# Optimization experiments

Measured on AMD Instinct MI355X. Metric: run time of the kernel, lower is better.

Reference implementation:

```python
import jax, jax.numpy as jnp
import numpy as np

N_NODES = 50000
N_EDGES = 800000
IN_CH = 128
HID = 128


def setup_inputs() -> dict:
    key = jax.random.key(0)
    ks = jax.random.split(key, 16)
    inp = {
        "x": jax.random.normal(ks[0], (N_NODES, IN_CH), dtype=jnp.float32),
        "edge_index": jax.random.randint(ks[1], (2, N_EDGES), 0, N_NODES, dtype=jnp.int64),
        "batch_size": 1024,
    }
    dims = [(IN_CH, HID), (HID, HID), (HID, HID)]
    for i, (din, dout) in enumerate(dims):
        s = 1.0 / np.sqrt(din)
        inp[f"W_l{i}"] = jax.random.uniform(ks[2 + 4 * i], (dout, din), jnp.float32, -s, s)
        inp[f"b_l{i}"] = jax.random.uniform(ks[3 + 4 * i], (dout,), jnp.float32, -s, s)
        inp[f"W_r{i}"] = jax.random.uniform(ks[4 + 4 * i], (dout, din), jnp.float32, -s, s)
        inp[f"a{i}"] = jnp.full((dout,), 0.25, dtype=jnp.float32)  # PReLU slope
    return inp


def _sage_prelu(x, src, dst, W_l, b_l, W_r, a):
    # mean aggregation of source messages at target nodes
    msg_sum = jax.ops.segment_sum(x[src], dst, num_segments=N_NODES)  # [N, din]
    deg = jax.ops.segment_sum(jnp.ones((src.shape[0],), x.dtype), dst, num_segments=N_NODES)
    agg = msg_sum / jnp.maximum(deg, 1.0)[:, None]
    out = agg @ W_l.T + b_l + x @ W_r.T  # lin_l(aggr) + lin_r(x), bias on lin_l only
    return jnp.where(out > 0, out, a * out)  # per-channel PReLU


def reference(x, edge_index, batch_size, W_l0, b_l0, W_r0, a0, W_l1, b_l1, W_r1, a1, W_l2, b_l2, W_r2, a2):
    src, dst = edge_index[0], edge_index[1]
    x = _sage_prelu(x, src, dst, W_l0, b_l0, W_r0, a0)
    x = _sage_prelu(x, src, dst, W_l1, b_l1, W_r1, a1)
    x = _sage_prelu(x, src, dst, W_l2, b_l2, W_r2, a2)
    return x[:batch_size]
```

## Files before the change

kernel.cpp:

```cpp
#include <hip/hip_runtime.h>

#define NN 50000
#define NE 800000
#define C 128
#define CAP 64
#define EB2 ((NE / 2 + 255) / 256)
#define SPLITB 1563
#define WB 96
#define EB4 ((NE / 4 + 255) / 256)
#define ASTRIDE 136

typedef __attribute__((ext_vector_type(8))) short bf16x8;
typedef __attribute__((ext_vector_type(4))) float f32x4;
typedef unsigned short ushort;

__device__ inline ushort bf16_rn(float f) {
    unsigned u = __builtin_bit_cast(unsigned, f);
    u += 0x7FFF + ((u >> 16) & 1);
    return (ushort)(u >> 16);
}
__device__ inline void split_bf16(float f, ushort& hi, ushort& lo) {
    hi = bf16_rn(f);
    float hif = __builtin_bit_cast(float, (unsigned)hi << 16);
    lo = bf16_rn(f - hif);
}
__device__ inline float bf_lo(unsigned u) { return __builtin_bit_cast(float, u << 16); }
__device__ inline float bf_hi(unsigned u) { return __builtin_bit_cast(float, u & 0xFFFF0000u); }


__global__ __launch_bounds__(256)
void prep_kernel(const int* __restrict__ dst, const float* __restrict__ x,
                 const float* __restrict__ W0, const float* __restrict__ W1,
                 const float* __restrict__ W2, const float* __restrict__ W3,
                 const float* __restrict__ W4, const float* __restrict__ W5,
                 int* __restrict__ deg, int* __restrict__ pos,
                 ushort* __restrict__ Ah, ushort* __restrict__ Al,
                 ushort* __restrict__ Wh, ushort* __restrict__ Wl) {
    int t = threadIdx.x;
    if (blockIdx.x < EB2) {
        int e0 = (blockIdx.x * 256 + t) * 2;
        if (e0 < NE) {
            int2 d2 = *(const int2*)(dst + e0);
            int p0 = atomicAdd(&deg[d2.x], 1);
            int p1 = atomicAdd(&deg[d2.y], 1);
            *(int2*)(pos + e0) = make_int2(p0, p1);
        }
    } else if (blockIdx.x < EB2 + SPLITB) {
        int tid = (blockIdx.x - EB2) * 256 + t;
        const int total = NN * C / 4;
        for (int i = tid; i < total; i += SPLITB * 256) {
            f32x4 v = ((const f32x4*)x)[i];
            ushort h0, h1, h2, h3, l0, l1, l2, l3;
            split_bf16(v.x, h0, l0);
            split_bf16(v.y, h1, l1);
            split_bf16(v.z, h2, l2);
            split_bf16(v.w, h3, l3);
            *(uint2*)(Ah + (size_t)i * 4) = make_uint2((unsigned)h0 | ((unsigned)h1 << 16),
                                                       (unsigned)h2 | ((unsigned)h3 << 16));
            *(uint2*)(Al + (size_t)i * 4) = make_uint2((unsigned)l0 | ((unsigned)l1 << 16),
                                                       (unsigned)l2 | ((unsigned)l3 << 16));
        }
    } else {
        const float* Ws[6] = {W0, W1, W2, W3, W4, W5};
        int i = (blockIdx.x - EB2 - SPLITB) * 256 + t;
        int mat = i >> 12;
        f32x4 v = ((const f32x4*)Ws[mat])[i & 4095];
        ushort h0, h1, h2, h3, l0, l1, l2, l3;
        split_bf16(v.x, h0, l0);
        split_bf16(v.y, h1, l1);
        split_bf16(v.z, h2, l2);
        split_bf16(v.w, h3, l3);
        *(uint2*)(Wh + (size_t)i * 4) = make_uint2((unsigned)h0 | ((unsigned)h1 << 16),
                                                   (unsigned)h2 | ((unsigned)h3 << 16));
        *(uint2*)(Wl + (size_t)i * 4) = make_uint2((unsigned)l0 | ((unsigned)l1 << 16),
                                                   (unsigned)l2 | ((unsigned)l3 << 16));
    }
}


__global__ __launch_bounds__(256)
void fill_kernel(const int* __restrict__ src, const int* __restrict__ dst,
                 const int* __restrict__ pos, int* __restrict__ col) {
    int e0 = (blockIdx.x * 256 + threadIdx.x) * 4;
    if (e0 >= NE) return;
    int4 da = *(const int4*)(dst + e0);
    int4 sa = *(const int4*)(src + e0);
    int4 pa = *(const int4*)(pos + e0);
    if (pa.x < CAP) col[da.x * CAP + pa.x] = sa.x;
    if (pa.y < CAP) col[da.y * CAP + pa.y] = sa.y;
    if (pa.z < CAP) col[da.z * CAP + pa.z] = sa.z;
    if (pa.w < CAP) col[da.w * CAP + pa.w] = sa.w;
}


__global__ __launch_bounds__(256)
void mark_kernel(const int* __restrict__ deg, const int* __restrict__ col,
                 int* __restrict__ needed, int rows_out) {
    int i = blockIdx.x * 256 + threadIdx.x;
    int n = i / CAP;
    int s = i - n * CAP;
    if (n >= rows_out) return;
    if (s == 0) needed[n] = 1;
    if (s < min(deg[n], CAP)) needed[col[n * CAP + s]] = 1;
}


__global__ __launch_bounds__(256)
void compact_kernel(const int* __restrict__ needed, int* __restrict__ list,
                    int* __restrict__ cnt) {
    int i = blockIdx.x * 256 + threadIdx.x;
    if (i < NN && needed[i]) {
        int p = atomicAdd(cnt, 1);
        list[p] = i;
    }
}


__global__ __launch_bounds__(256)
void agg_kernel(const ushort* __restrict__ xh, const int* __restrict__ deg,
                const int* __restrict__ col,
                const int* __restrict__ list, const int* __restrict__ countp,
                ushort* __restrict__ aggh, ushort* __restrict__ aggl, int nodes) {
    int i = (blockIdx.x * blockDim.x + threadIdx.x) >> 6;
    int lane = threadIdx.x & 63;
    int cnt = list ? *countp : nodes;
    if (i >= cnt) return;
    int node = list ? list[i] : i;
    int quad = lane >> 4;
    int ql   = lane & 15;
    int d = min(deg[node], CAP);
    int start = node * CAP;
    int end = start + d;
    const uint4* xr = (const uint4*)xh;
    float a0=0,a1=0,a2=0,a3=0,a4=0,a5=0,a6=0,a7=0;
    int e = start;
    for (; e + 7 < end; e += 8) {
        int i0 = col[e + quad];
        int i1 = col[e + 4 + quad];
        uint4 u0 = xr[(size_t)i0 * 16 + ql];
        uint4 u1 = xr[(size_t)i1 * 16 + ql];
        a0 += bf_lo(u0.x) + bf_lo(u1.x); a1 += bf_hi(u0.x) + bf_hi(u1.x);
        a2 += bf_lo(u0.y) + bf_lo(u1.y); a3 += bf_hi(u0.y) + bf_hi(u1.y);
        a4 += bf_lo(u0.z) + bf_lo(u1.z); a5 += bf_hi(u0.z) + bf_hi(u1.z);
        a6 += bf_lo(u0.w) + bf_lo(u1.w); a7 += bf_hi(u0.w) + bf_hi(u1.w);
    }
    for (; e + 3 < end; e += 4) {
        uint4 u = xr[(size_t)col[e + quad] * 16 + ql];
        a0 += bf_lo(u.x); a1 += bf_hi(u.x);
        a2 += bf_lo(u.y); a3 += bf_hi(u.y);
        a4 += bf_lo(u.z); a5 += bf_hi(u.z);
        a6 += bf_lo(u.w); a7 += bf_hi(u.w);
    }
    int rem = end - e;
    if (quad < rem) {
        uint4 u = xr[(size_t)col[e + quad] * 16 + ql];
        a0 += bf_lo(u.x); a1 += bf_hi(u.x);
        a2 += bf_lo(u.y); a3 += bf_hi(u.y);
        a4 += bf_lo(u.z); a5 += bf_hi(u.z);
        a6 += bf_lo(u.w); a7 += bf_hi(u.w);
    }
    a0 += __shfl_xor(a0, 16, 64); a0 += __shfl_xor(a0, 32, 64);
    a1 += __shfl_xor(a1, 16, 64); a1 += __shfl_xor(a1, 32, 64);
    a2 += __shfl_xor(a2, 16, 64); a2 += __shfl_xor(a2, 32, 64);
    a3 += __shfl_xor(a3, 16, 64); a3 += __shfl_xor(a3, 32, 64);
    a4 += __shfl_xor(a4, 16, 64); a4 += __shfl_xor(a4, 32, 64);
    a5 += __shfl_xor(a5, 16, 64); a5 += __shfl_xor(a5, 32, 64);
    a6 += __shfl_xor(a6, 16, 64); a6 += __shfl_xor(a6, 32, 64);
    a7 += __shfl_xor(a7, 16, 64); a7 += __shfl_xor(a7, 32, 64);
    if (quad == 0) {
        float inv = 1.0f / (float)max(d, 1);
        float m[8] = {a0*inv, a1*inv, a2*inv, a3*inv, a4*inv, a5*inv, a6*inv, a7*inv};
        ushort h[8], o[8];
        #pragma unroll
        for (int j = 0; j < 8; ++j) split_bf16(m[j], h[j], o[j]);
        size_t off = (size_t)node * C + ql * 8;
        *(uint4*)(aggh + off) = make_uint4((unsigned)h[0] | ((unsigned)h[1] << 16),
                                           (unsigned)h[2] | ((unsigned)h[3] << 16),
                                           (unsigned)h[4] | ((unsigned)h[5] << 16),
                                           (unsigned)h[6] | ((unsigned)h[7] << 16));
        *(uint4*)(aggl + off) = make_uint4((unsigned)o[0] | ((unsigned)o[1] << 16),
                                           (unsigned)o[2] | ((unsigned)o[3] << 16),
                                           (unsigned)o[4] | ((unsigned)o[5] << 16),
                                           (unsigned)o[6] | ((unsigned)o[7] << 16));
    }
}


__global__ __launch_bounds__(256, 3)
void gemm_kernel(const ushort* __restrict__ Ah, const ushort* __restrict__ Al,
                 const ushort* __restrict__ Xh, const ushort* __restrict__ Xl,
                 const ushort* __restrict__ Wlh, const ushort* __restrict__ Wll,
                 const ushort* __restrict__ Wrh, const ushort* __restrict__ Wrl,
                 const float* __restrict__ bl, const float* __restrict__ slope,
                 const int* __restrict__ list, const int* __restrict__ countp,
                 float* __restrict__ outf, ushort* __restrict__ outh,
                 ushort* __restrict__ outl, int rows) {
    __shared__ ushort Ahi[64 * ASTRIDE];
    __shared__ ushort Alo[64 * ASTRIDE];
    int t = threadIdx.x;
    int lane = t & 63;
    int w = t >> 6;
    int l = lane & 15;
    int q = lane >> 4;
    int row0 = blockIdx.x * 64;
    int cnt = list ? min(*countp, rows) : rows;
    if (row0 >= cnt) return;

    f32x4 acc[4][2];
    #pragma unroll
    for (int mt = 0; mt < 4; ++mt)
        #pragma unroll
        for (int nt = 0; nt < 2; ++nt)
            acc[mt][nt] = (f32x4){0.f, 0.f, 0.f, 0.f};

    #pragma unroll
    for (int mat = 0; mat < 2; ++mat) {
        const ushort* WH = mat ? Wrh : Wlh;
        const ushort* WL = mat ? Wrl : Wll;
        const ushort* Ph = mat ? Xh : Ah;
        const ushort* Pl = mat ? Xl : Al;

        bf16x8 bhi[2][4], blo[2][4];
        #pragma unroll
        for (int nt = 0; nt < 2; ++nt) {
            int n = w * 32 + nt * 16 + l;
            const ushort* wp = WH + (size_t)n * C + q * 8;
            const ushort* wq = WL + (size_t)n * C + q * 8;
            #pragma unroll
            for (int kb = 0; kb < 4; ++kb) {
                bhi[nt][kb] = *(const bf16x8*)(wp + kb * 32);
                blo[nt][kb] = *(const bf16x8*)(wq + kb * 32);
            }
        }

        __syncthreads();
        int ar = t >> 2;
        int aq = t & 3;
        int ridx = min(row0 + ar, cnt - 1);
        int r = list ? list[ridx] : ridx;
        ushort* dh = Ahi + ar * ASTRIDE + aq * 32;
        ushort* dl = Alo + ar * ASTRIDE + aq * 32;
        const ushort* ph = Ph + (size_t)r * C + aq * 32;
        const ushort* pl = Pl + (size_t)r * C + aq * 32;
        #pragma unroll
        for (int i = 0; i < 4; ++i) {
            *(uint4*)(dh + i * 8) = *(const uint4*)(ph + i * 8);
            *(uint4*)(dl + i * 8) = *(const uint4*)(pl + i * 8);
        }
        __syncthreads();

        #pragma unroll
        for (int kb = 0; kb < 4; ++kb) {
            #pragma unroll
            for (int mt = 0; mt < 4; ++mt) {
                int off = (mt * 16 + l) * ASTRIDE + kb * 32 + q * 8;
                bf16x8 ahi = *(const bf16x8*)(Ahi + off);
                bf16x8 alo = *(const bf16x8*)(Alo + off);
                #pragma unroll
                for (int nt = 0; nt < 2; ++nt) {
                    acc[mt][nt] = __builtin_amdgcn_mfma_f32_16x16x32_bf16(ahi, bhi[nt][kb], acc[mt][nt], 0, 0, 0);
                    acc[mt][nt] = __builtin_amdgcn_mfma_f32_16x16x32_bf16(alo, bhi[nt][kb], acc[mt][nt], 0, 0, 0);
                    acc[mt][nt] = __builtin_amdgcn_mfma_f32_16x16x32_bf16(ahi, blo[nt][kb], acc[mt][nt], 0, 0, 0);
                }
            }
        }
    }

    #pragma unroll
    for (int nt = 0; nt < 2; ++nt) {
        int n = w * 32 + nt * 16 + l;
        float b = bl[n], s = slope[n];
        #pragma unroll
        for (int mt = 0; mt < 4; ++mt) {
            #pragma unroll
            for (int rg = 0; rg < 4; ++rg) {
                int ridx = row0 + mt * 16 + q * 4 + rg;
                if (ridx < cnt) {
                    int r = list ? list[ridx] : ridx;
                    float v = acc[mt][nt][rg] + b;
                    v = v > 0.f ? v : s * v;
                    if (outf) {
                        outf[(size_t)r * C + n] = v;
                    } else {
                        ushort hh, ll;
                        split_bf16(v, hh, ll);
                        outh[(size_t)r * C + n] = hh;
                        outl[(size_t)r * C + n] = ll;
                    }
                }
            }
        }
    }
}


extern "C" void kernel_launch(void* const* d_in, const int* in_sizes, int n_in,
                              void* d_out, int out_size, void* d_ws, size_t ws_size,
                              hipStream_t stream) {
    const float* x   = (const float*)d_in[0];
    const int*   src = (const int*)d_in[1];
    const int*   dst = src + NE;
    const float* Wl[3] = {(const float*)d_in[3], (const float*)d_in[7],  (const float*)d_in[11]};
    const float* bl[3] = {(const float*)d_in[4], (const float*)d_in[8],  (const float*)d_in[12]};
    const float* Wr[3] = {(const float*)d_in[5], (const float*)d_in[9],  (const float*)d_in[13]};
    const float* sl[3] = {(const float*)d_in[6], (const float*)d_in[10], (const float*)d_in[14]};

    int*   deg     = (int*)d_ws;
    int*   needed  = deg + 50016;
    int*   cnt     = needed + 50016;
    int*   pos     = cnt + 16;
    int*   col     = pos + 800000;
    int*   list    = col + NN * CAP;
    ushort* Whs    = (ushort*)(list + 50016);
    ushort* Wls    = Whs + 6 * 16384;
    ushort* Gh     = Wls + 6 * 16384;
    ushort* Gl     = Gh + (size_t)NN * C;
    ushort* Ah     = Gl + (size_t)NN * C;
    ushort* Al     = Ah + (size_t)NN * C;
    ushort* Bh     = Al + (size_t)NN * C;
    ushort* Bl     = Bh + (size_t)NN * C;

    int rows_out = out_size / C;

    hipMemsetAsync(deg, 0, (2 * 50016 + 16) * sizeof(int), stream);

    prep_kernel<<<EB2 + SPLITB + WB, 256, 0, stream>>>(
        dst, x, Wl[0], Wr[0], Wl[1], Wr[1], Wl[2], Wr[2],
        deg, pos, Ah, Al, Whs, Wls);
    fill_kernel<<<EB4, 256, 0, stream>>>(src, dst, pos, col);

    mark_kernel<<<(rows_out * CAP + 255) / 256, 256, 0, stream>>>(deg, col, needed, rows_out);
    compact_kernel<<<(NN + 255) / 256, 256, 0, stream>>>(needed, list, cnt);

    agg_kernel<<<(NN + 3) / 4, 256, 0, stream>>>(Ah, deg, col, nullptr, nullptr, Gh, Gl, NN);
    gemm_kernel<<<(NN + 63) / 64, 256, 0, stream>>>(Gh, Gl, Ah, Al,
                                                    Whs + 0 * 16384, Wls + 0 * 16384,
                                                    Whs + 1 * 16384, Wls + 1 * 16384,
                                                    bl[0], sl[0], nullptr, nullptr,
                                                    nullptr, Bh, Bl, NN);

    agg_kernel<<<(NN + 3) / 4, 256, 0, stream>>>(Bh, deg, col, list, cnt, Gh, Gl, NN);
    gemm_kernel<<<(NN + 63) / 64, 256, 0, stream>>>(Gh, Gl, Bh, Bl,
                                                    Whs + 2 * 16384, Wls + 2 * 16384,
                                                    Whs + 3 * 16384, Wls + 3 * 16384,
                                                    bl[1], sl[1], list, cnt,
                                                    nullptr, Ah, Al, NN);

    agg_kernel<<<(rows_out + 3) / 4, 256, 0, stream>>>(Ah, deg, col, nullptr, nullptr,
                                                       Gh, Gl, rows_out);
    gemm_kernel<<<(rows_out + 63) / 64, 256, 0, stream>>>(Gh, Gl, Ah, Al,
                                                          Whs + 4 * 16384, Wls + 4 * 16384,
                                                          Whs + 5 * 16384, Wls + 5 * 16384,
                                                          bl[2], sl[2], nullptr, nullptr,
                                                          (float*)d_out, nullptr, nullptr,
                                                          rows_out);
}
```

Before: 292.9 us.

## Fold needed-node marking and compaction into prep and fill kernels

Marks the source nodes needed by output rows directly from the edge list inside the prep kernel, and moves list compaction into extra blocks of the fill kernel. This removes two separate kernel launches and the dependency on the filled adjacency for marking. Marking scans all edges instead of only output rows' adjacency, and ignores the CAP truncation, so the needed set may be a superset. The GEMM launch bound also rises from 3 to 4 waves per SIMD, which may force register spills.

```diff
diff --git a/kernel.cpp b/kernel.cpp
--- a/kernel.cpp
+++ b/kernel.cpp
@@ -7,7 +7,9 @@
 #define EB2 ((NE / 2 + 255) / 256)
 #define SPLITB 1563
 #define WB 96
+#define MB4 ((NE / 4 + 255) / 256)
 #define EB4 ((NE / 4 + 255) / 256)
+#define CB  ((NN + 255) / 256)
 #define ASTRIDE 136
 
 typedef __attribute__((ext_vector_type(8))) short bf16x8;
@@ -29,13 +31,15 @@
 
 
 __global__ __launch_bounds__(256)
-void prep_kernel(const int* __restrict__ dst, const float* __restrict__ x,
+void prep_kernel(const int* __restrict__ src, const int* __restrict__ dst,
+                 const float* __restrict__ x,
                  const float* __restrict__ W0, const float* __restrict__ W1,
                  const float* __restrict__ W2, const float* __restrict__ W3,
                  const float* __restrict__ W4, const float* __restrict__ W5,
                  int* __restrict__ deg, int* __restrict__ pos,
                  ushort* __restrict__ Ah, ushort* __restrict__ Al,
-                 ushort* __restrict__ Wh, ushort* __restrict__ Wl) {
+                 ushort* __restrict__ Wh, ushort* __restrict__ Wl,
+                 int* __restrict__ needed, int rows_out) {
     int t = threadIdx.x;
     if (blockIdx.x < EB2) {
         int e0 = (blockIdx.x * 256 + t) * 2;
@@ -60,7 +64,7 @@
             *(uint2*)(Al + (size_t)i * 4) = make_uint2((unsigned)l0 | ((unsigned)l1 << 16),
                                                        (unsigned)l2 | ((unsigned)l3 << 16));
         }
-    } else {
+    } else if (blockIdx.x < EB2 + SPLITB + WB) {
         const float* Ws[6] = {W0, W1, W2, W3, W4, W5};
         int i = (blockIdx.x - EB2 - SPLITB) * 256 + t;
         int mat = i >> 12;
@@ -74,44 +78,42 @@
                                                    (unsigned)h2 | ((unsigned)h3 << 16));
         *(uint2*)(Wl + (size_t)i * 4) = make_uint2((unsigned)l0 | ((unsigned)l1 << 16),
                                                    (unsigned)l2 | ((unsigned)l3 << 16));
+    } else {
+        int e0 = ((blockIdx.x - EB2 - SPLITB - WB) * 256 + t) * 4;
+        if (e0 < NE) {
+            int4 da = *(const int4*)(dst + e0);
+            int4 sa = *(const int4*)(src + e0);
+            if (da.x < rows_out) needed[sa.x] = 1;
+            if (da.y < rows_out) needed[sa.y] = 1;
+            if (da.z < rows_out) needed[sa.z] = 1;
+            if (da.w < rows_out) needed[sa.w] = 1;
+        }
     }
 }
 
 
 __global__ __launch_bounds__(256)
 void fill_kernel(const int* __restrict__ src, const int* __restrict__ dst,
-                 const int* __restrict__ pos, int* __restrict__ col) {
-    int e0 = (blockIdx.x * 256 + threadIdx.x) * 4;
-    if (e0 >= NE) return;
-    int4 da = *(const int4*)(dst + e0);
-    int4 sa = *(const int4*)(src + e0);
-    int4 pa = *(const int4*)(pos + e0);
-    if (pa.x < CAP) col[da.x * CAP + pa.x] = sa.x;
-    if (pa.y < CAP) col[da.y * CAP + pa.y] = sa.y;
-    if (pa.z < CAP) col[da.z * CAP + pa.z] = sa.z;
-    if (pa.w < CAP) col[da.w * CAP + pa.w] = sa.w;
-}
-
-
-__global__ __launch_bounds__(256)
-void mark_kernel(const int* __restrict__ deg, const int* __restrict__ col,
-                 int* __restrict__ needed, int rows_out) {
-    int i = blockIdx.x * 256 + threadIdx.x;
-    int n = i / CAP;
-    int s = i - n * CAP;
-    if (n >= rows_out) return;
-    if (s == 0) needed[n] = 1;
-    if (s < min(deg[n], CAP)) needed[col[n * CAP + s]] = 1;
-}
-
-
-__global__ __launch_bounds__(256)
-void compact_kernel(const int* __restrict__ needed, int* __restrict__ list,
-                    int* __restrict__ cnt) {
-    int i = blockIdx.x * 256 + threadIdx.x;
-    if (i < NN && needed[i]) {
-        int p = atomicAdd(cnt, 1);
-        list[p] = i;
+                 const int* __restrict__ pos, int* __restrict__ col,
+                 const int* __restrict__ needed, int* __restrict__ list,
+                 int* __restrict__ cnt, int rows_out) {
+    int t = threadIdx.x;
+    if (blockIdx.x < EB4) {
+        int e0 = (blockIdx.x * 256 + t) * 4;
+        if (e0 >= NE) return;
+        int4 da = *(const int4*)(dst + e0);
+        int4 sa = *(const int4*)(src + e0);
+        int4 pa = *(const int4*)(pos + e0);
+        if (pa.x < CAP) col[da.x * CAP + pa.x] = sa.x;
+        if (pa.y < CAP) col[da.y * CAP + pa.y] = sa.y;
+        if (pa.z < CAP) col[da.z * CAP + pa.z] = sa.z;
+        if (pa.w < CAP) col[da.w * CAP + pa.w] = sa.w;
+    } else {
+        int i = (blockIdx.x - EB4) * 256 + t;
+        if (i < NN && (i < rows_out || needed[i])) {
+            int p = atomicAdd(cnt, 1);
+            list[p] = i;
+        }
     }
 }
 
@@ -186,7 +188,7 @@
 }
 
 
-__global__ __launch_bounds__(256, 3)
+__global__ __launch_bounds__(256, 4)
 void gemm_kernel(const ushort* __restrict__ Ah, const ushort* __restrict__ Al,
                  const ushort* __restrict__ Xh, const ushort* __restrict__ Xl,
                  const ushort* __restrict__ Wlh, const ushort* __restrict__ Wll,
@@ -324,13 +326,10 @@
 
     hipMemsetAsync(deg, 0, (2 * 50016 + 16) * sizeof(int), stream);
 
-    prep_kernel<<<EB2 + SPLITB + WB, 256, 0, stream>>>(
-        dst, x, Wl[0], Wr[0], Wl[1], Wr[1], Wl[2], Wr[2],
-        deg, pos, Ah, Al, Whs, Wls);
-    fill_kernel<<<EB4, 256, 0, stream>>>(src, dst, pos, col);
-
-    mark_kernel<<<(rows_out * CAP + 255) / 256, 256, 0, stream>>>(deg, col, needed, rows_out);
-    compact_kernel<<<(NN + 255) / 256, 256, 0, stream>>>(needed, list, cnt);
+    prep_kernel<<<EB2 + SPLITB + WB + MB4, 256, 0, stream>>>(
+        src, dst, x, Wl[0], Wr[0], Wl[1], Wr[1], Wl[2], Wr[2],
+        deg, pos, Ah, Al, Whs, Wls, needed, rows_out);
+    fill_kernel<<<EB4 + CB, 256, 0, stream>>>(src, dst, pos, col, needed, list, cnt, rows_out);
 
     agg_kernel<<<(NN + 3) / 4, 256, 0, stream>>>(Ah, deg, col, nullptr, nullptr, Gh, Gl, NN);
     gemm_kernel<<<(NN + 63) / 64, 256, 0, stream>>>(Gh, Gl, Ah, Al,
```

Result: faster. 285.1 us (-2.7%).
